# Optimization experiments

Hardware: AMD Instinct MI355X
Metric: run time of the kernel (lower is better)

Reference implementation:

```python
import jax, jax.numpy as jnp
import numpy as np

B, T, W, D = 2, 64, 32, 512
H = 8                      # n_heads
N = 64                     # d_state
EXPAND = 2
DIN = EXPAND * D           # 1024 d_inner
R = -(-D // 16)            # dt_rank = ceil(d_model/16) = 32
K = 4                      # d_conv (mamba default)


def setup_inputs():
    key = jax.random.key(0)
    ks = jax.random.split(key, 20)
    s = 0.02
    inp = {
        'x': jax.random.normal(ks[0], (B, T, W, D), jnp.float32),
        'wq': jax.random.normal(ks[1], (D, D), jnp.float32) * s,
        'bq': jnp.zeros((D,), jnp.float32),
        'wk': jax.random.normal(ks[2], (D, D), jnp.float32) * s,
        'bk': jnp.zeros((D,), jnp.float32),
        'wv': jax.random.normal(ks[3], (D, D), jnp.float32) * s,
        'bv': jnp.zeros((D,), jnp.float32),
        'wo': jax.random.normal(ks[4], (D, D), jnp.float32) * s,
        'bo': jnp.zeros((D,), jnp.float32),
        'in_proj_w': jax.random.normal(ks[5], (2 * DIN, D), jnp.float32) * s,
        'conv_w': jax.random.normal(ks[6], (DIN, 1, K), jnp.float32) * 0.2,
        'conv_b': jnp.zeros((DIN,), jnp.float32),
        'x_proj_w': jax.random.normal(ks[7], (R + 2 * N, DIN), jnp.float32) * s,
        'dt_proj_w': jax.random.normal(ks[8], (DIN, R), jnp.float32) * 0.1,
        'dt_proj_b': jnp.full((DIN,), -4.6, jnp.float32),  # ~softplus^-1(0.01)
        'A_log': jnp.log(jnp.broadcast_to(jnp.arange(1, N + 1, dtype=jnp.float32), (DIN, N))),
        'D_param': jnp.ones((DIN,), jnp.float32),
        'out_proj_w': jax.random.normal(ks[9], (D, DIN), jnp.float32) * s,
        'ln_w': jnp.ones((D,), jnp.float32),
        'ln_b': jnp.zeros((D,), jnp.float32),
    }
    return inp


def _attention(xf, wq, bq, wk, bk, wv, bv, wo, bo):
    b, L, d = xf.shape
    e = d // H
    q = (xf @ wq.T + bq).reshape(b, L, H, e)
    k = (xf @ wk.T + bk).reshape(b, L, H, e)
    v = (xf @ wv.T + bv).reshape(b, L, H, e)
    scale = 1.0 / jnp.sqrt(jnp.float32(e))
    scores = jnp.einsum('blhe,bshe->bhls', q, k) * scale
    causal = jnp.tril(jnp.ones((L, L), bool))
    scores = jnp.where(causal, scores, jnp.finfo(scores.dtype).min)
    attn = jax.nn.softmax(scores, axis=-1)  # dropout off (eval mode)
    out = jnp.einsum('bhls,bshe->blhe', attn, v).reshape(b, L, d)
    return out @ wo.T + bo


def _mamba(xf, in_proj_w, conv_w, conv_b, x_proj_w, dt_proj_w, dt_proj_b,
           A_log, D_param, out_proj_w):
    b, L, d = xf.shape
    xz = xf @ in_proj_w.T                 # (B,L,2*DIN)
    x_in, z = jnp.split(xz, 2, axis=-1)
    # causal depthwise conv1d over L
    xc = jnp.transpose(x_in, (0, 2, 1))   # (B,DIN,L)
    xc = jax.lax.conv_general_dilated(
        xc, conv_w, window_strides=(1,), padding=[(K - 1, 0)],
        feature_group_count=DIN, dimension_numbers=('NCH', 'OIH', 'NCH'))
    xc = xc + conv_b[None, :, None]
    u = jax.nn.silu(jnp.transpose(xc, (0, 2, 1)))   # (B,L,DIN)
    dbc = u @ x_proj_w.T                             # (B,L,R+2N)
    dt, Bm, Cm = dbc[..., :R], dbc[..., R:R + N], dbc[..., R + N:]
    dt = jax.nn.softplus(dt @ dt_proj_w.T + dt_proj_b)  # (B,L,DIN)
    A = -jnp.exp(A_log)                                 # (DIN,N)

    def step(h, t):
        dt_t, B_t, C_t, u_t = t  # (b,DIN),(b,N),(b,N),(b,DIN)
        dA = jnp.exp(dt_t[..., None] * A)                       # (b,DIN,N)
        h = dA * h + (dt_t * u_t)[..., None] * B_t[:, None, :]  # (b,DIN,N)
        y = jnp.einsum('bdn,bn->bd', h, C_t)
        return h, y

    h0 = jnp.zeros((b, DIN, N), xf.dtype)
    xs = (jnp.swapaxes(dt, 0, 1), jnp.swapaxes(Bm, 0, 1),
          jnp.swapaxes(Cm, 0, 1), jnp.swapaxes(u, 0, 1))
    _, ys = jax.lax.scan(step, h0, xs)
    y = jnp.swapaxes(ys, 0, 1) + u * D_param   # (B,L,DIN)
    y = y * jax.nn.silu(z)
    return y @ out_proj_w.T


def reference(x, wq, bq, wk, bk, wv, bv, wo, bo, in_proj_w, conv_w, conv_b,
              x_proj_w, dt_proj_w, dt_proj_b, A_log, D_param, out_proj_w,
              ln_w, ln_b):
    b, t, w, d = x.shape
    L = t * w
    xf = x.reshape(b, L, d)
    x_attn = _attention(xf, wq, bq, wk, bk, wv, bv, wo, bo).reshape(b, t, w, d)
    x_mamba = _mamba(xf, in_proj_w, conv_w, conv_b, x_proj_w, dt_proj_w,
                     dt_proj_b, A_log, D_param, out_proj_w).reshape(b, t, w, d)
    h = x + x_attn + x_mamba
    mu = jnp.mean(h, axis=-1, keepdims=True)
    var = jnp.mean(jnp.square(h - mu), axis=-1, keepdims=True)
    return (h - mu) * jax.lax.rsqrt(var + 1e-5) * ln_w + ln_b
```

## Files before the change

kernel.cpp:

```cpp
#include <hip/hip_runtime.h>

typedef __attribute__((ext_vector_type(4))) float f32x4;
typedef __attribute__((ext_vector_type(8))) short short8;
typedef __attribute__((ext_vector_type(2))) unsigned uint2e;

#define DEV static __device__ __forceinline__

DEV ushort f2b(float f) {
  union { float f; unsigned u; } v; v.f = f;
  unsigned r = v.u + 0x7FFF + ((v.u >> 16) & 1);
  return (ushort)(r >> 16);
}
DEV unsigned pack_bf2(float lo, float hi) {
  return (unsigned)f2b(lo) | ((unsigned)f2b(hi) << 16);
}
DEV float bflo(unsigned p) { return __uint_as_float(p << 16); }
DEV float bfhi(unsigned p) { return __uint_as_float(p & 0xFFFF0000u); }
DEV float b2f(ushort u) { return __uint_as_float((unsigned)u << 16); }

DEV float fexp2(float x) { float r; asm("v_exp_f32 %0, %1" : "=v"(r) : "v"(x)); return r; }

DEV float xor32_add_lo(float s) {
  uint2e r = __builtin_amdgcn_permlane32_swap(__float_as_uint(s), __float_as_uint(s), false, false);
  return s + __uint_as_float(r.x);
}

#define QP(x, ctrl) __int_as_float(__builtin_amdgcn_update_dpp(0, __float_as_int(x), (ctrl), 0xf, 0xf, false))
#define SWZ(x, off) __int_as_float(__builtin_amdgcn_ds_swizzle(__float_as_int(x), (off)))
#define DPP_ADD(x, ctrl, rmask) \
  ((x) + __int_as_float(__builtin_amdgcn_update_dpp(0, __float_as_int(x), (ctrl), (rmask), 0xf, false)))

#define LOG2E 1.44269504f

#define BB    2
#define LL    2048
#define DD    512
#define HH    8
#define EE    64
#define DIN   1024
#define NS    64
#define RR    32
#define BL    4096
#define NCH   16
#define TC    128
#define NC    1536
#define NQ    3584
#define XOFF  1536
#define ZOFF  2560
#define MFMA(a,b,c) __builtin_amdgcn_mfma_f32_16x16x32_bf16((a),(b),(c),0,0,0)

struct CvtJobs {
  const float* src[7];
  ushort*      dst[7];
  int          n[7];
};

__global__ __launch_bounds__(256) void cvt_multi(CvtJobs j) {
  int job = blockIdx.y;
  const float* s = j.src[job];
  ushort* d = j.dst[job];
  int n = j.n[job];
  for (int i = blockIdx.x * 256 + threadIdx.x; i < n; i += gridDim.x * 256)
    d[i] = f2b(s[i]);
}

__global__ __launch_bounds__(256) void pack_wcomb(
    const float* __restrict__ wo, const float* __restrict__ opw,
    const float* __restrict__ bq, const float* __restrict__ bk,
    const float* __restrict__ bv, ushort* __restrict__ wc,
    float* __restrict__ bqi)
{
  int i = blockIdx.x * 256 + threadIdx.x;
  if (i < NQ)
    bqi[i] = (i < DD) ? bq[i] : (i < 2 * DD) ? bk[i - DD] : (i < NC) ? bv[i - 2 * DD] : 0.f;
  if (i >= DD * NC) return;
  int n = i / NC, c = i - n * NC;
  float v = (c < DD) ? wo[n * DD + c] : opw[n * DIN + (c - DD)];
  wc[i] = f2b(v);
}

__global__ __launch_bounds__(256) void gemm_bt(
    const ushort* __restrict__ A, const ushort* __restrict__ W,
    const float* __restrict__ bias, float* __restrict__ outF,
    ushort* __restrict__ outB, int M, int N, int K, int act)
{
  __shared__ ushort As[64][40];
  __shared__ ushort Ws[64][40];
  int m0 = blockIdx.y * 64, n0 = blockIdx.x * 64;
  int tid = threadIdx.x, l = tid & 63, w = tid >> 6;
  int wm = (w >> 1) * 32, wn = (w & 1) * 32;
  int lr = l & 15, kl = (l >> 4) * 8;
  int srow = tid >> 2, sk = (tid & 3) * 8;
  f32x4 acc[2][2] = {};

  for (int k0 = 0; k0 < K; k0 += 32) {
    uint4 av = *(const uint4*)&A[(size_t)(m0 + srow) * K + k0 + sk];
    uint4 wv;
    if (n0 + srow < N) wv = *(const uint4*)&W[(size_t)(n0 + srow) * K + k0 + sk];
    else { wv.x = 0; wv.y = 0; wv.z = 0; wv.w = 0; }
    *(uint4*)&As[srow][sk] = av;
    *(uint4*)&Ws[srow][sk] = wv;
    __syncthreads();
    short8 a0 = *(const short8*)&As[wm + lr][kl];
    short8 a1 = *(const short8*)&As[wm + 16 + lr][kl];
    short8 b0 = *(const short8*)&Ws[wn + lr][kl];
    short8 b1 = *(const short8*)&Ws[wn + 16 + lr][kl];
    acc[0][0] = MFMA(a0, b0, acc[0][0]);
    acc[0][1] = MFMA(a0, b1, acc[0][1]);
    acc[1][0] = MFMA(a1, b0, acc[1][0]);
    acc[1][1] = MFMA(a1, b1, acc[1][1]);
    __syncthreads();
  }

  #pragma unroll
  for (int mi = 0; mi < 2; mi++)
    #pragma unroll
    for (int ni = 0; ni < 2; ni++) {
      int rbase = m0 + wm + mi * 16 + ((l >> 4) << 2);
      int col = n0 + wn + ni * 16 + lr;
      if (col < N) {
        float bval = bias ? bias[col] : 0.f;
        #pragma unroll
        for (int r = 0; r < 4; r++) {
          float v = acc[mi][ni][r] + bval;
          if (act == 1) v = (v > 20.f) ? v : log1pf(__expf(v));
          size_t o = (size_t)(rbase + r) * N + col;
          if (outF) outF[o] = v;
          if (outB) outB[o] = f2b(v);
        }
      }
    }
}

__global__ __launch_bounds__(256) void gemm128(
    const ushort* __restrict__ A, const ushort* __restrict__ W,
    const float* __restrict__ bias, float* __restrict__ outF,
    ushort* __restrict__ outB, int M, int N, int K)
{
  __shared__ ushort As[128][40];
  __shared__ ushort Ws[128][40];
  int tid = threadIdx.x, l = tid & 63, w = tid >> 6;
  int m0 = blockIdx.y * 128, n0 = blockIdx.x * 128;
  int wm = (w >> 1) * 64, wn = (w & 1) * 64;
  int lr = l & 15, kl = (l >> 4) * 8;
  int srow = tid >> 1, sk = (tid & 1) * 16;
  f32x4 acc[4][4] = {};

  const ushort* Ap = A + (size_t)(m0 + srow) * K + sk;
  const ushort* Wp = W + (size_t)(n0 + srow) * K + sk;

  for (int k0 = 0; k0 < K; k0 += 32) {
    uint4 a0 = *(const uint4*)(Ap);
    uint4 a1 = *(const uint4*)(Ap + 8);
    uint4 b0 = *(const uint4*)(Wp);
    uint4 b1 = *(const uint4*)(Wp + 8);
    __syncthreads();
    *(uint4*)&As[srow][sk]     = a0;
    *(uint4*)&As[srow][sk + 8] = a1;
    *(uint4*)&Ws[srow][sk]     = b0;
    *(uint4*)&Ws[srow][sk + 8] = b1;
    __syncthreads();
    short8 af[4], bf[4];
    #pragma unroll
    for (int mi = 0; mi < 4; mi++) af[mi] = *(const short8*)&As[wm + mi * 16 + lr][kl];
    #pragma unroll
    for (int ni = 0; ni < 4; ni++) bf[ni] = *(const short8*)&Ws[wn + ni * 16 + lr][kl];
    #pragma unroll
    for (int mi = 0; mi < 4; mi++)
      #pragma unroll
      for (int ni = 0; ni < 4; ni++)
        acc[mi][ni] = MFMA(af[mi], bf[ni], acc[mi][ni]);
    Ap += 32; Wp += 32;
  }

  #pragma unroll
  for (int mi = 0; mi < 4; mi++)
    #pragma unroll
    for (int ni = 0; ni < 4; ni++) {
      int rbase = m0 + wm + mi * 16 + ((l >> 4) << 2);
      int col = n0 + wn + ni * 16 + lr;
      float bval = bias ? bias[col] : 0.f;
      #pragma unroll
      for (int r = 0; r < 4; r++) {
        float v = acc[mi][ni][r] + bval;
        size_t o = (size_t)(rbase + r) * N + col;
        if (outF) outF[o] = v;
        if (outB) outB[o] = f2b(v);
      }
    }
}

__global__ __launch_bounds__(256) void attn_xproj(
    const ushort* __restrict__ qkv, ushort* __restrict__ comb,
    const ushort* __restrict__ ub, const ushort* __restrict__ xpw,
    float* __restrict__ dbc)
{
  __shared__ ushort smem[4 * 64 * 72];
  int id = blockIdx.x;
  int tid = threadIdx.x, l = tid & 63, w = tid >> 6;

  if (id < 512) {
    typedef ushort row72[72];
    row72* Qs = (row72*)smem;
    row72* Ks = Qs + 64;
    row72* Vt = Ks + 64;
    row72* Ps = Vt + 64;
    int qt = 31 - (id & 31), h = (id >> 5) & 7, b = id >> 8;
    int w16 = w * 16, lr = l & 15, kl = (l >> 4) * 8;

    for (int i = tid; i < 512; i += 256) {
      int row = i >> 3, c8 = (i & 7) * 8;
      *(uint4*)&Qs[row][c8] =
          *(const uint4*)&qkv[((size_t)(b * LL + qt * 64 + row)) * NQ + h * EE + c8];
    }
    __syncthreads();

    float l_r[4] = {0.f, 0.f, 0.f, 0.f};
    f32x4 oacc[4] = {};
    const float SSC = 0.125f * LOG2E;

    for (int kv = 0; kv <= qt; kv++) {
      for (int i = tid; i < 512; i += 256) {
        int s = i >> 3, c8 = (i & 7) * 8;
        size_t rb = ((size_t)(b * LL + kv * 64 + s)) * NQ + h * EE + c8;
        *(uint4*)&Ks[s][c8] = *(const uint4*)&qkv[rb + DD];
        uint4 vv = *(const uint4*)&qkv[rb + 2 * DD];
        const ushort* pv = (const ushort*)&vv;
        #pragma unroll
        for (int jj = 0; jj < 8; jj++) Vt[c8 + jj][s] = pv[jj];
      }
      __syncthreads();

      f32x4 sacc[4] = {};
      #pragma unroll
      for (int kk = 0; kk < 2; kk++) {
        short8 aq = *(const short8*)&Qs[w16 + lr][kk * 32 + kl];
        #pragma unroll
        for (int nt = 0; nt < 4; nt++) {
          short8 bk8 = *(const short8*)&Ks[nt * 16 + lr][kk * 32 + kl];
          sacc[nt] = MFMA(aq, bk8, sacc[nt]);
        }
      }

      bool diag = (kv == qt);
      #pragma unroll
      for (int r = 0; r < 4; r++) {
        int rloc = w16 + ((l >> 4) << 2) + r;
        float rs = 0.f;
        #pragma unroll
        for (int nt = 0; nt < 4; nt++) {
          float v = sacc[nt][r] * SSC;
          if (diag && (nt * 16 + lr) > rloc) v = -1e30f;
          float p = fexp2(v);
          rs += p;
          Ps[rloc][nt * 16 + lr] = f2b(p);
        }
        rs += QP(rs, 0xB1);
        rs += QP(rs, 0x4E);
        rs += SWZ(rs, 0x101F);
        rs += SWZ(rs, 0x201F);
        l_r[r] += rs;
      }

      #pragma unroll
      for (int kk = 0; kk < 2; kk++) {
        short8 ap = *(const short8*)&Ps[w16 + lr][kk * 32 + kl];
        #pragma unroll
        for (int nt = 0; nt < 4; nt++) {
          short8 bv8 = *(const short8*)&Vt[nt * 16 + lr][kk * 32 + kl];
          oacc[nt] = MFMA(ap, bv8, oacc[nt]);
        }
      }
      __syncthreads();
    }

    #pragma unroll
    for (int nt = 0; nt < 4; nt++)
      #pragma unroll
      for (int r = 0; r < 4; r++) {
        int row = qt * 64 + w16 + ((l >> 4) << 2) + r;
        float v = oacc[nt][r] / l_r[r];
        comb[((size_t)(b * LL + row)) * NC + h * EE + nt * 16 + lr] = f2b(v);
      }
  } else {
    typedef ushort row40[40];
    row40* As = (row40*)smem;
    row40* Ws = As + 64;
    int rid = id - 512;
    int n0 = (rid % 3) * 64, m0 = (rid / 3) * 64;
    int wm = (w >> 1) * 32, wn = (w & 1) * 32;
    int lr = l & 15, kl = (l >> 4) * 8;
    int srow = tid >> 2, sk = (tid & 3) * 8;
    f32x4 acc[2][2] = {};

    for (int k0 = 0; k0 < DIN; k0 += 32) {
      uint4 av = *(const uint4*)&ub[(size_t)(m0 + srow) * DIN + k0 + sk];
      uint4 wv;
      if (n0 + srow < 160) wv = *(const uint4*)&xpw[(size_t)(n0 + srow) * DIN + k0 + sk];
      else { wv.x = 0; wv.y = 0; wv.z = 0; wv.w = 0; }
      *(uint4*)&As[srow][sk] = av;
      *(uint4*)&Ws[srow][sk] = wv;
      __syncthreads();
      short8 a0 = *(const short8*)&As[wm + lr][kl];
      short8 a1 = *(const short8*)&As[wm + 16 + lr][kl];
      short8 b0 = *(const short8*)&Ws[wn + lr][kl];
      short8 b1 = *(const short8*)&Ws[wn + 16 + lr][kl];
      acc[0][0] = MFMA(a0, b0, acc[0][0]);
      acc[0][1] = MFMA(a0, b1, acc[0][1]);
      acc[1][0] = MFMA(a1, b0, acc[1][0]);
      acc[1][1] = MFMA(a1, b1, acc[1][1]);
      __syncthreads();
    }

    #pragma unroll
    for (int mi = 0; mi < 2; mi++)
      #pragma unroll
      for (int ni = 0; ni < 2; ni++) {
        int rbase = m0 + wm + mi * 16 + ((l >> 4) << 2);
        int col = n0 + wn + ni * 16 + lr;
        if (col < 160) {
          #pragma unroll
          for (int r = 0; r < 4; r++)
            dbc[(size_t)(rbase + r) * 160 + col] = acc[mi][ni][r];
        }
      }
  }
}

__global__ __launch_bounds__(256) void conv_silu(
    const ushort* __restrict__ xz, const float* __restrict__ cw,
    const float* __restrict__ cb, ushort* __restrict__ ub)
{
  int i = blockIdx.x * 256 + threadIdx.x;
  int d = i & (DIN - 1);
  int r = i >> 10;
  int t0 = (r & (LL / 8 - 1)) * 8;
  int b = r >> 8;
  float c0 = cw[d * 4], c1 = cw[d * 4 + 1], c2 = cw[d * 4 + 2], c3 = cw[d * 4 + 3];
  float bias = cb[d];
  float xw[11];
  #pragma unroll
  for (int j = 0; j < 3; j++) {
    int tt = t0 - 3 + j;
    xw[j] = (tt >= 0) ? b2f(xz[((size_t)(b * LL + tt)) * NQ + XOFF + d]) : 0.f;
  }
  #pragma unroll
  for (int j = 0; j < 8; j++)
    xw[3 + j] = b2f(xz[((size_t)(b * LL + t0 + j)) * NQ + XOFF + d]);
  size_t obase = (size_t)(b * LL + t0) * DIN + d;
  #pragma unroll
  for (int j = 0; j < 8; j++) {
    float s = bias + xw[j] * c0 + xw[j + 1] * c1 + xw[j + 2] * c2 + xw[j + 3] * c3;
    ub[obase + (size_t)j * DIN] = f2b(s / (1.f + __expf(-s)));
  }
}

__global__ __launch_bounds__(256) void dt_bc(
    const float* __restrict__ dbc, const ushort* __restrict__ dtw,
    const float* __restrict__ dtb, ushort* __restrict__ dt_b,
    unsigned* __restrict__ bbp, float4* __restrict__ bcp4)
{
  __shared__ ushort As[64][40];
  __shared__ ushort Ws[64][40];
  int id = blockIdx.x;
  int tid = threadIdx.x;
  if (id < 1024) {
    int m0 = (id >> 4) * 64, n0 = (id & 15) * 64;
    int l = tid & 63, w = tid >> 6;
    int wm = (w >> 1) * 32, wn = (w & 1) * 32;
    int lr = l & 15, kl = (l >> 4) * 8;
    int srow = tid >> 2, sk = (tid & 3) * 8;

    const float* ar = dbc + (size_t)(m0 + srow) * 160 + sk;
    short8 av;
    #pragma unroll
    for (int j = 0; j < 8; j++) ((ushort*)&av)[j] = f2b(ar[j]);
    *(short8*)&As[srow][sk] = av;
    *(uint4*)&Ws[srow][sk] = *(const uint4*)&dtw[(size_t)(n0 + srow) * RR + sk];
    __syncthreads();

    f32x4 acc[2][2] = {};
    short8 a0 = *(const short8*)&As[wm + lr][kl];
    short8 a1 = *(const short8*)&As[wm + 16 + lr][kl];
    short8 b0 = *(const short8*)&Ws[wn + lr][kl];
    short8 b1 = *(const short8*)&Ws[wn + 16 + lr][kl];
    acc[0][0] = MFMA(a0, b0, acc[0][0]);
    acc[0][1] = MFMA(a0, b1, acc[0][1]);
    acc[1][0] = MFMA(a1, b0, acc[1][0]);
    acc[1][1] = MFMA(a1, b1, acc[1][1]);

    #pragma unroll
    for (int mi = 0; mi < 2; mi++)
      #pragma unroll
      for (int ni = 0; ni < 2; ni++) {
        int rbase = m0 + wm + mi * 16 + ((l >> 4) << 2);
        int col = n0 + wn + ni * 16 + lr;
        float bval = dtb[col];
        #pragma unroll
        for (int r = 0; r < 4; r++) {
          float v = acc[mi][ni][r] + bval;
          v = (v > 20.f) ? v : log1pf(__expf(v));
          dt_b[(size_t)(rbase + r) * DIN + col] = f2b(v);
        }
      }
  } else {
    int i = (id - 1024) * 256 + tid;
    int n = i & 63, tp = (i >> 6) & 1023, b = i >> 16;
    size_t r0 = ((size_t)(b * LL + 2 * tp)) * 160;
    float B0 = dbc[r0 + 32 + n],  C0 = dbc[r0 + 96 + n];
    float B1 = dbc[r0 + 192 + n], C1 = dbc[r0 + 256 + n];
    bbp[i] = pack_bf2(B0, B1);
    bcp4[i] = make_float4(B0, C0, B1, C1);
  }
}

__global__ __launch_bounds__(256) void pack_dtu(
    const ushort* __restrict__ dtb16, const ushort* __restrict__ ub,
    const ushort* __restrict__ xz, const float* __restrict__ dpar,
    unsigned* __restrict__ dtu_p, unsigned* __restrict__ sg_p)
{
  __shared__ float s_dt[32][65], s_du[32][65], s_gz[32][65], s_ug[32][65];
  int d0 = blockIdx.x * 64, t0 = blockIdx.y * 32;
  int tid = threadIdx.x;
  int c = tid & 63, r4 = tid >> 6;
  float Dv = dpar[d0 + c];
  #pragma unroll
  for (int k = 0; k < 8; k++) {
    int r = k * 4 + r4;
    size_t row = (size_t)(t0 + r);
    float dtv = b2f(dtb16[row * DIN + d0 + c]);
    float uv  = b2f(ub   [row * DIN + d0 + c]);
    float zz  = b2f(xz   [row * NQ + ZOFF + d0 + c]);
    float g = zz / (1.f + __expf(-zz));
    s_dt[r][c] = dtv;
    s_du[r][c] = dtv * uv;
    s_gz[r][c] = g;
    s_ug[r][c] = uv * Dv * g;
  }
  __syncthreads();
  int dl = tid >> 2, q = tid & 3;
  int b = t0 >> 11, tl0 = t0 & (LL - 1);
  size_t obase = ((size_t)(b * DIN + d0 + dl)) * LL + tl0 + q * 8;
  #pragma unroll
  for (int tt = 0; tt < 8; tt++) {
    int t = q * 8 + tt;
    dtu_p[obase + tt] = pack_bf2(s_dt[t][dl], s_du[t][dl]);
    sg_p [obase + tt] = pack_bf2(s_gz[t][dl], s_ug[t][dl]);
  }
}

__global__ __launch_bounds__(256) void scan_phase1(
    const unsigned* __restrict__ dtu_p, const unsigned* __restrict__ bbp,
    const float* __restrict__ alog, float* __restrict__ hf, float* __restrict__ ap)
{
  __shared__ float lds[4][TC][2];
  int tid = threadIdx.x, w = tid >> 6, l = tid & 63;
  int wid = blockIdx.x * 4 + w;
  int d = wid & (DIN - 1);
  int c = (wid >> 10) & (NCH - 1);
  int b = wid >> 14;
  float An2 = -__expf(alog[d * NS + l]) * LOG2E;

  size_t pbase = ((size_t)(b * DIN + d)) * LL + c * TC;
  unsigned p0 = dtu_p[pbase + l];
  unsigned p1 = dtu_p[pbase + 64 + l];
  float s0 = bflo(p0), s1 = bflo(p1);
  s0 = DPP_ADD(s0, 0x111, 0xf); s0 = DPP_ADD(s0, 0x112, 0xf);
  s0 = DPP_ADD(s0, 0x114, 0xf); s0 = DPP_ADD(s0, 0x118, 0xf);
  s0 = DPP_ADD(s0, 0x142, 0xa); s0 = DPP_ADD(s0, 0x143, 0xc);
  s1 = DPP_ADD(s1, 0x111, 0xf); s1 = DPP_ADD(s1, 0x112, 0xf);
  s1 = DPP_ADD(s1, 0x114, 0xf); s1 = DPP_ADD(s1, 0x118, 0xf);
  s1 = DPP_ADD(s1, 0x142, 0xa); s1 = DPP_ADD(s1, 0x143, 0xc);
  float T0 = __uint_as_float(__builtin_amdgcn_readlane(__float_as_uint(s0), 63));
  float T  = T0 + __uint_as_float(__builtin_amdgcn_readlane(__float_as_uint(s1), 63));
  lds[w][l][0]      = T - s0;
  lds[w][l][1]      = bfhi(p0);
  lds[w][64 + l][0] = (T - T0) - s1;
  lds[w][64 + l][1] = bfhi(p1);
  __syncthreads();

  const unsigned* bq = bbp + ((size_t)(b * 1024 + c * 64) * 64 + l);
  float h0 = 0.f, h1 = 0.f;
  for (int g = 0; g < 16; g++) {
    unsigned bv[4];
    #pragma unroll
    for (int k = 0; k < 4; k++) bv[k] = bq[k * 64];
    const float* gb = &lds[w][g * 8][0];
    #pragma unroll
    for (int j = 0; j < 8; j++) {
      float2 dd = *(const float2*)(gb + j * 2);
      float Bv = (j & 1) ? bfhi(bv[j >> 1]) : bflo(bv[j >> 1]);
      float a = fexp2(dd.x * An2);
      if (j & 1) h1 += a * (dd.y * Bv);
      else       h0 += a * (dd.y * Bv);
    }
    bq += 256;
  }
  size_t o = (((size_t)((b << 10) + d) * NCH) + c) * 64 + l;
  hf[o] = h0 + h1;
  ap[o] = fexp2(T * An2);
}

__global__ __launch_bounds__(256) void scan_carry(
    const float* __restrict__ hf, const float* __restrict__ ap,
    float* __restrict__ carry)
{
  int i = blockIdx.x * 256 + threadIdx.x;
  int n = i & 63;
  int d = (i >> 6) & (DIN - 1);
  int b = i >> 16;
  size_t base = ((size_t)((b << 10) + d) * NCH) * 64 + n;
  float cur = 0.f;
  #pragma unroll
  for (int c = 0; c < NCH; c++) {
    carry[base + (size_t)c * 64] = cur;
    cur = ap[base + (size_t)c * 64] * cur + hf[base + (size_t)c * 64];
  }
}

__global__ __launch_bounds__(256) void scan_phase3(
    const unsigned* __restrict__ dtu_p, const unsigned* __restrict__ sg_p,
    const float4* __restrict__ bcp4, const float* __restrict__ alog,
    const float* __restrict__ carry, ushort* __restrict__ ymt)
{
  __shared__ float lds[4][TC][4];
  __shared__ ushort yt[4][TC];
  int tid = threadIdx.x, w = tid >> 6, l = tid & 63;
  int wid = blockIdx.x * 4 + w;
  int d = wid & (DIN - 1);
  int c = (wid >> 10) & (NCH - 1);
  int b = wid >> 14;
  float An2 = -__expf(alog[d * NS + l]) * LOG2E;

  size_t pbase = ((size_t)(b * DIN + d)) * LL + c * TC;
  #pragma unroll
  for (int q = 0; q < 2; q++) {
    unsigned pd = dtu_p[pbase + q * 64 + l];
    unsigned pg = sg_p [pbase + q * 64 + l];
    lds[w][q * 64 + l][0] = bflo(pd);
    lds[w][q * 64 + l][1] = bfhi(pd);
    lds[w][q * 64 + l][2] = bflo(pg);
    lds[w][q * 64 + l][3] = bfhi(pg);
  }
  __syncthreads();

  float h = carry[(((size_t)((b << 10) + d) * NCH) + c) * 64 + l];
  const float4* bq = bcp4 + ((size_t)(b * 1024 + c * 64) * 64 + l);
  bool s1f = l & 1, s2f = l & 2, s4f = l & 4;
  bool wl = l < 8;

  for (int g = 0; g < 16; g++) {
    float4 bcs[4];
    bcs[0] = bq[0]; bcs[1] = bq[64]; bcs[2] = bq[128]; bcs[3] = bq[192];
    const float* gb = &lds[w][g * 8][0];
    float p[8];
    #pragma unroll
    for (int j = 0; j < 8; j++) {
      float2 dd = *(const float2*)(gb + j * 4);
      float Bv = (j & 1) ? bcs[j >> 1].z : bcs[j >> 1].x;
      float Cv = (j & 1) ? bcs[j >> 1].w : bcs[j >> 1].y;
      float a = fexp2(dd.x * An2);
      h = a * h + dd.y * Bv;
      p[j] = h * Cv;
    }
    #pragma unroll
    for (int j = 0; j < 8; j++) p[j] += QP(p[j], 0xB1);
    float q0 = s1f ? p[1] : p[0];
    float q1 = s1f ? p[3] : p[2];
    float q2 = s1f ? p[5] : p[4];
    float q3 = s1f ? p[7] : p[6];
    q0 += QP(q0, 0x4E); q1 += QP(q1, 0x4E);
    q2 += QP(q2, 0x4E); q3 += QP(q3, 0x4E);
    float r0 = s2f ? q1 : q0;
    float r1 = s2f ? q3 : q2;
    r0 += SWZ(r0, 0x101F); r1 += SWZ(r1, 0x101F);
    float s = s4f ? r1 : r0;
    s += QP(s, 0x128);
    s += SWZ(s, 0x401F);
    s = xor32_add_lo(s);

    float2 sgv = *(const float2*)(&lds[w][g * 8 + (l & 7)][2]);
    if (wl) yt[w][g * 8 + l] = f2b(s * sgv.x + sgv.y);
    bq += 256;
  }
  __syncthreads();
  unsigned vv = *(const unsigned*)&yt[w][2 * l];
  ((unsigned*)(ymt + pbase))[l] = vv;
}

__global__ __launch_bounds__(256) void transpose_ym(
    const ushort* __restrict__ ymt, ushort* __restrict__ comb)
{
  __shared__ ushort tile[64][72];
  int tid = threadIdx.x;
  int bx = blockIdx.x;
  int by = blockIdx.y;
  int b  = blockIdx.z;
  int r = tid >> 2, c16 = (tid & 3) * 16;
  const ushort* src = ymt + ((size_t)(b * DIN + bx * 64 + r)) * LL + by * 64 + c16;
  *(uint4*)&tile[r][c16]     = *(const uint4*)src;
  *(uint4*)&tile[r][c16 + 8] = *(const uint4*)(src + 8);
  __syncthreads();
  ushort tmp[16];
  #pragma unroll
  for (int j = 0; j < 16; j++) tmp[j] = tile[c16 + j][r];
  ushort* dst = comb + ((size_t)(b * LL + by * 64 + r)) * NC + DD + bx * 64 + c16;
  *(uint4*)dst       = *(uint4*)&tmp[0];
  *(uint4*)(dst + 8) = *(uint4*)&tmp[8];
}

__global__ __launch_bounds__(256) void residual_ln(
    const float* __restrict__ x, const float* __restrict__ so,
    const float* __restrict__ lw, const float* __restrict__ lb,
    float* __restrict__ out)
{
  int row = blockIdx.x * 4 + (threadIdx.x >> 6);
  int l = threadIdx.x & 63;
  size_t base = (size_t)row * DD;
  float h[8];
  float s = 0.f, s2 = 0.f;
  #pragma unroll
  for (int half = 0; half < 2; half++) {
    int c = half * 256 + l * 4;
    float4 xv = *(const float4*)(x + base + c);
    float4 sv = *(const float4*)(so + base + c);
    float* hp = h + half * 4;
    hp[0] = xv.x + sv.x;
    hp[1] = xv.y + sv.y;
    hp[2] = xv.z + sv.z;
    hp[3] = xv.w + sv.w;
    #pragma unroll
    for (int j = 0; j < 4; j++) { s += hp[j]; s2 += hp[j] * hp[j]; }
  }
  #pragma unroll
  for (int o = 1; o < 64; o <<= 1) { s += __shfl_xor(s, o); s2 += __shfl_xor(s2, o); }
  float mean = s * (1.f / DD);
  float var = s2 * (1.f / DD) - mean * mean;
  float rs = rsqrtf(var + 1e-5f);
  #pragma unroll
  for (int half = 0; half < 2; half++) {
    int c = half * 256 + l * 4;
    float4 ov;
    ov.x = (h[half*4+0] - mean) * rs * lw[c+0] + lb[c+0];
    ov.y = (h[half*4+1] - mean) * rs * lw[c+1] + lb[c+1];
    ov.z = (h[half*4+2] - mean) * rs * lw[c+2] + lb[c+2];
    ov.w = (h[half*4+3] - mean) * rs * lw[c+3] + lb[c+3];
    *(float4*)(out + base + c) = ov;
  }
}

extern "C" void kernel_launch(void* const* d_in, const int* in_sizes, int n_in,
                              void* d_out, int out_size, void* d_ws, size_t ws_size,
                              hipStream_t stream) {
  const float* x    = (const float*)d_in[0];
  const float* wq   = (const float*)d_in[1];
  const float* bq   = (const float*)d_in[2];
  const float* wk   = (const float*)d_in[3];
  const float* bk   = (const float*)d_in[4];
  const float* wv   = (const float*)d_in[5];
  const float* bv   = (const float*)d_in[6];
  const float* wo   = (const float*)d_in[7];
  const float* bo   = (const float*)d_in[8];
  const float* inw  = (const float*)d_in[9];
  const float* cw   = (const float*)d_in[10];
  const float* cb   = (const float*)d_in[11];
  const float* xpw  = (const float*)d_in[12];
  const float* dtw  = (const float*)d_in[13];
  const float* dtb  = (const float*)d_in[14];
  const float* alog = (const float*)d_in[15];
  const float* dpar = (const float*)d_in[16];
  const float* opw  = (const float*)d_in[17];
  const float* lnw  = (const float*)d_in[18];
  const float* lnb  = (const float*)d_in[19];

  char* ws = (char*)d_ws;
  size_t off = 0;
  auto alloc = [&](size_t bytes) -> void* {
    void* p = ws + off;
    off += (bytes + 255) & ~(size_t)255;
    return p;
  };

  const size_t BLD = (size_t)BL * DD;
  const size_t BLDIN = (size_t)BL * DIN;

  ushort* xf_b   = (ushort*)alloc(BLD * 2);
  ushort* wqi_b  = (ushort*)alloc((size_t)NQ * DD * 2);
  float*  bqi    = (float*)alloc(NQ * 4);
  ushort* xpw_b  = (ushort*)alloc(160 * DIN * 2);
  ushort* dtw_b  = (ushort*)alloc(DIN * RR * 2);
  ushort* wcomb_b= (ushort*)alloc((size_t)DD * NC * 2);
  ushort* qkvxz_b= (ushort*)alloc((size_t)BL * NQ * 2);
  ushort* comb_a = (ushort*)alloc((size_t)BL * NC * 2);
  float*  sum_o  = (float*)alloc(BLD * 4);
  ushort* u_b    = (ushort*)alloc(BLDIN * 2);
  float*  dbc    = (float*)alloc((size_t)BL * 160 * 4);
  ushort* dt_b   = (ushort*)alloc(BLDIN * 2);
  ushort* ymt_b  = (ushort*)alloc(BLDIN * 2);
  unsigned* bbp  = (unsigned*)alloc((size_t)BB * (LL / 2) * NS * 4);
  float4* bcp4   = (float4*)alloc((size_t)BB * (LL / 2) * NS * sizeof(float4));
  unsigned* dtu_p = (unsigned*)alloc(BLDIN * 4);
  unsigned* sg_p  = (unsigned*)alloc(BLDIN * 4);

  const size_t SCN = (size_t)BB * DIN * NCH * 64;
  float* hf_s    = (float*)qkvxz_b;
  float* ap_s    = hf_s + SCN;
  float* carry_s = (float*)alloc(SCN * 4);

  CvtJobs cj;
  cj.src[0] = x;    cj.dst[0] = xf_b;                cj.n[0] = (int)BLD;
  cj.src[1] = wq;   cj.dst[1] = wqi_b;               cj.n[1] = DD * DD;
  cj.src[2] = wk;   cj.dst[2] = wqi_b + DD * DD;     cj.n[2] = DD * DD;
  cj.src[3] = wv;   cj.dst[3] = wqi_b + 2 * DD * DD; cj.n[3] = DD * DD;
  cj.src[4] = inw;  cj.dst[4] = wqi_b + 3 * DD * DD; cj.n[4] = 2 * DIN * DD;
  cj.src[5] = xpw;  cj.dst[5] = xpw_b;               cj.n[5] = 160 * DIN;
  cj.src[6] = dtw;  cj.dst[6] = dtw_b;               cj.n[6] = DIN * RR;
  cvt_multi<<<dim3(256, 7), 256, 0, stream>>>(cj);
  pack_wcomb<<<dim3((DD * NC + 255) / 256), 256, 0, stream>>>(wo, opw, bq, bk, bv, wcomb_b, bqi);

  gemm128<<<dim3(28, 32), 256, 0, stream>>>(xf_b, wqi_b, bqi, nullptr, qkvxz_b, BL, NQ, DD);

  conv_silu<<<dim3(2048), 256, 0, stream>>>(qkvxz_b, cw, cb, u_b);

  attn_xproj<<<dim3(704), 256, 0, stream>>>(qkvxz_b, comb_a, u_b, xpw_b, dbc);

  dt_bc<<<dim3(1536), 256, 0, stream>>>(dbc, dtw_b, dtb, dt_b, bbp, bcp4);

  pack_dtu<<<dim3(16, 128), 256, 0, stream>>>(dt_b, u_b, qkvxz_b, dpar, dtu_p, sg_p);
  scan_phase1<<<dim3(8192), 256, 0, stream>>>(dtu_p, bbp, alog, hf_s, ap_s);
  scan_carry<<<dim3(512), 256, 0, stream>>>(hf_s, ap_s, carry_s);
  scan_phase3<<<dim3(8192), 256, 0, stream>>>(dtu_p, sg_p, bcp4, alog, carry_s, ymt_b);
  transpose_ym<<<dim3(16, 32, BB), 256, 0, stream>>>(ymt_b, comb_a);

  gemm_bt<<<dim3(8, 64), 256, 0, stream>>>(comb_a, wcomb_b, bo, sum_o, nullptr, BL, DD, NC, 0);

  residual_ln<<<dim3(1024), 256, 0, stream>>>(x, sum_o, lnw, lnb, (float*)d_out);
}
```

Before: 346.3 us.

## Fuse dt packing into dt_bc GEMM and merge scan phase1 with carry

The dt projection kernel now packs dt, dt*u, the silu gate and the D-skip term directly from its tile through shared memory and writes the transposed packed buffers. This removes the separate pack_dtu kernel and the bf16 dt_b round trip. Scan phase 1 and the carry propagation are merged into one kernel per (batch, channel) that keeps chunk states in LDS, which drops the hf/ap global buffers and one launch. The trade-offs are lower parallelism in phase 1 (2048 blocks, each wave doing 4 chunks serially) and more LDS per block in dt_bc.

```diff
diff --git a/kernel.cpp b/kernel.cpp
--- a/kernel.cpp
+++ b/kernel.cpp
@@ -357,15 +357,20 @@
 
 __global__ __launch_bounds__(256) void dt_bc(
     const float* __restrict__ dbc, const ushort* __restrict__ dtw,
-    const float* __restrict__ dtb, ushort* __restrict__ dt_b,
+    const float* __restrict__ dtb, const float* __restrict__ dpar,
+    const ushort* __restrict__ ub, const ushort* __restrict__ xz,
+    unsigned* __restrict__ dtu_p, unsigned* __restrict__ sg_p,
     unsigned* __restrict__ bbp, float4* __restrict__ bcp4)
 {
   __shared__ ushort As[64][40];
   __shared__ ushort Ws[64][40];
+  __shared__ unsigned s_a[64][65];
+  __shared__ unsigned s_b[64][65];
   int id = blockIdx.x;
   int tid = threadIdx.x;
   if (id < 1024) {
     int m0 = (id >> 4) * 64, n0 = (id & 15) * 64;
+    int b = m0 >> 11, t0g = m0 & (LL - 1);
     int l = tid & 63, w = tid >> 6;
     int wm = (w >> 1) * 32, wn = (w & 1) * 32;
     int lr = l & 15, kl = (l >> 4) * 8;
@@ -393,16 +398,49 @@
     for (int mi = 0; mi < 2; mi++)
       #pragma unroll
       for (int ni = 0; ni < 2; ni++) {
-        int rbase = m0 + wm + mi * 16 + ((l >> 4) << 2);
-        int col = n0 + wn + ni * 16 + lr;
-        float bval = dtb[col];
+        int rl = wm + mi * 16 + ((l >> 4) << 2);
+        int cl = wn + ni * 16 + lr;
+        float bval = dtb[n0 + cl];
         #pragma unroll
         for (int r = 0; r < 4; r++) {
           float v = acc[mi][ni][r] + bval;
           v = (v > 20.f) ? v : log1pf(__expf(v));
-          dt_b[(size_t)(rbase + r) * DIN + col] = f2b(v);
+          s_a[rl + r][cl] = __float_as_uint(v);
         }
       }
+    __syncthreads();
+
+    {
+      int c = tid & 63, r4 = tid >> 6;
+      float Dv = dpar[n0 + c];
+      #pragma unroll
+      for (int k = 0; k < 16; k++) {
+        int r = k * 4 + r4;
+        float dtv = __uint_as_float(s_a[r][c]);
+        float uv  = b2f(ub[(size_t)(m0 + r) * DIN + n0 + c]);
+        float zz  = b2f(xz[(size_t)(m0 + r) * NQ + ZOFF + n0 + c]);
+        float g = zz / (1.f + __expf(-zz));
+        s_a[r][c] = pack_bf2(dtv, dtv * uv);
+        s_b[r][c] = pack_bf2(g, uv * Dv * g);
+      }
+    }
+    __syncthreads();
+
+    {
+      int dl = tid >> 2, q = tid & 3;
+      unsigned vd[16], vs[16];
+      #pragma unroll
+      for (int j = 0; j < 16; j++) {
+        vd[j] = s_a[q * 16 + j][dl];
+        vs[j] = s_b[q * 16 + j][dl];
+      }
+      size_t obase = ((size_t)(b * DIN + n0 + dl)) * LL + t0g + q * 16;
+      #pragma unroll
+      for (int jj = 0; jj < 4; jj++) {
+        *(uint4*)&dtu_p[obase + jj * 4] = *(uint4*)&vd[jj * 4];
+        *(uint4*)&sg_p [obase + jj * 4] = *(uint4*)&vs[jj * 4];
+      }
+    }
   } else {
     int i = (id - 1024) * 256 + tid;
     int n = i & 63, tp = (i >> 6) & 1023, b = i >> 16;
@@ -414,108 +452,70 @@
   }
 }
 
-__global__ __launch_bounds__(256) void pack_dtu(
-    const ushort* __restrict__ dtb16, const ushort* __restrict__ ub,
-    const ushort* __restrict__ xz, const float* __restrict__ dpar,
-    unsigned* __restrict__ dtu_p, unsigned* __restrict__ sg_p)
-{
-  __shared__ float s_dt[32][65], s_du[32][65], s_gz[32][65], s_ug[32][65];
-  int d0 = blockIdx.x * 64, t0 = blockIdx.y * 32;
-  int tid = threadIdx.x;
-  int c = tid & 63, r4 = tid >> 6;
-  float Dv = dpar[d0 + c];
-  #pragma unroll
-  for (int k = 0; k < 8; k++) {
-    int r = k * 4 + r4;
-    size_t row = (size_t)(t0 + r);
-    float dtv = b2f(dtb16[row * DIN + d0 + c]);
-    float uv  = b2f(ub   [row * DIN + d0 + c]);
-    float zz  = b2f(xz   [row * NQ + ZOFF + d0 + c]);
-    float g = zz / (1.f + __expf(-zz));
-    s_dt[r][c] = dtv;
-    s_du[r][c] = dtv * uv;
-    s_gz[r][c] = g;
-    s_ug[r][c] = uv * Dv * g;
+__global__ __launch_bounds__(256) void scan_p1c(
+    const unsigned* __restrict__ dtu_p, const unsigned* __restrict__ bbp,
+    const float* __restrict__ alog, float* __restrict__ carry)
+{
+  __shared__ float ldsE[4][TC][2];
+  __shared__ float hfL[NCH][NS];
+  __shared__ float apL[NCH][NS];
+  int tid = threadIdx.x, w = tid >> 6, l = tid & 63;
+  int bid = blockIdx.x;
+  int d = bid & (DIN - 1);
+  int b = bid >> 10;
+  float An2 = -__expf(alog[d * NS + l]) * LOG2E;
+
+  for (int k = 0; k < 4; k++) {
+    int cc = w * 4 + k;
+    size_t pbase = ((size_t)(b * DIN + d)) * LL + cc * TC;
+    unsigned p0 = dtu_p[pbase + l];
+    unsigned p1 = dtu_p[pbase + 64 + l];
+    float s0 = bflo(p0), s1 = bflo(p1);
+    s0 = DPP_ADD(s0, 0x111, 0xf); s0 = DPP_ADD(s0, 0x112, 0xf);
+    s0 = DPP_ADD(s0, 0x114, 0xf); s0 = DPP_ADD(s0, 0x118, 0xf);
+    s0 = DPP_ADD(s0, 0x142, 0xa); s0 = DPP_ADD(s0, 0x143, 0xc);
+    s1 = DPP_ADD(s1, 0x111, 0xf); s1 = DPP_ADD(s1, 0x112, 0xf);
+    s1 = DPP_ADD(s1, 0x114, 0xf); s1 = DPP_ADD(s1, 0x118, 0xf);
+    s1 = DPP_ADD(s1, 0x142, 0xa); s1 = DPP_ADD(s1, 0x143, 0xc);
+    float T0 = __uint_as_float(__builtin_amdgcn_readlane(__float_as_uint(s0), 63));
+    float T  = T0 + __uint_as_float(__builtin_amdgcn_readlane(__float_as_uint(s1), 63));
+    ldsE[w][l][0]      = T - s0;
+    ldsE[w][l][1]      = bfhi(p0);
+    ldsE[w][64 + l][0] = (T - T0) - s1;
+    ldsE[w][64 + l][1] = bfhi(p1);
+
+    const unsigned* bq = bbp + ((size_t)(b * 1024 + cc * 64) * 64 + l);
+    float h0 = 0.f, h1 = 0.f;
+    for (int g = 0; g < 16; g++) {
+      unsigned bv[4];
+      #pragma unroll
+      for (int kk = 0; kk < 4; kk++) bv[kk] = bq[kk * 64];
+      const float* gb = &ldsE[w][g * 8][0];
+      #pragma unroll
+      for (int j = 0; j < 8; j++) {
+        float2 dd = *(const float2*)(gb + j * 2);
+        float Bv = (j & 1) ? bfhi(bv[j >> 1]) : bflo(bv[j >> 1]);
+        float a = fexp2(dd.x * An2);
+        if (j & 1) h1 += a * (dd.y * Bv);
+        else       h0 += a * (dd.y * Bv);
+      }
+      bq += 256;
+    }
+    hfL[cc][l] = h0 + h1;
+    apL[cc][l] = fexp2(T * An2);
   }
   __syncthreads();
-  int dl = tid >> 2, q = tid & 3;
-  int b = t0 >> 11, tl0 = t0 & (LL - 1);
-  size_t obase = ((size_t)(b * DIN + d0 + dl)) * LL + tl0 + q * 8;
-  #pragma unroll
-  for (int tt = 0; tt < 8; tt++) {
-    int t = q * 8 + tt;
-    dtu_p[obase + tt] = pack_bf2(s_dt[t][dl], s_du[t][dl]);
-    sg_p [obase + tt] = pack_bf2(s_gz[t][dl], s_ug[t][dl]);
-  }
-}
-
-__global__ __launch_bounds__(256) void scan_phase1(
-    const unsigned* __restrict__ dtu_p, const unsigned* __restrict__ bbp,
-    const float* __restrict__ alog, float* __restrict__ hf, float* __restrict__ ap)
-{
-  __shared__ float lds[4][TC][2];
-  int tid = threadIdx.x, w = tid >> 6, l = tid & 63;
-  int wid = blockIdx.x * 4 + w;
-  int d = wid & (DIN - 1);
-  int c = (wid >> 10) & (NCH - 1);
-  int b = wid >> 14;
-  float An2 = -__expf(alog[d * NS + l]) * LOG2E;
-
-  size_t pbase = ((size_t)(b * DIN + d)) * LL + c * TC;
-  unsigned p0 = dtu_p[pbase + l];
-  unsigned p1 = dtu_p[pbase + 64 + l];
-  float s0 = bflo(p0), s1 = bflo(p1);
-  s0 = DPP_ADD(s0, 0x111, 0xf); s0 = DPP_ADD(s0, 0x112, 0xf);
-  s0 = DPP_ADD(s0, 0x114, 0xf); s0 = DPP_ADD(s0, 0x118, 0xf);
-  s0 = DPP_ADD(s0, 0x142, 0xa); s0 = DPP_ADD(s0, 0x143, 0xc);
-  s1 = DPP_ADD(s1, 0x111, 0xf); s1 = DPP_ADD(s1, 0x112, 0xf);
-  s1 = DPP_ADD(s1, 0x114, 0xf); s1 = DPP_ADD(s1, 0x118, 0xf);
-  s1 = DPP_ADD(s1, 0x142, 0xa); s1 = DPP_ADD(s1, 0x143, 0xc);
-  float T0 = __uint_as_float(__builtin_amdgcn_readlane(__float_as_uint(s0), 63));
-  float T  = T0 + __uint_as_float(__builtin_amdgcn_readlane(__float_as_uint(s1), 63));
-  lds[w][l][0]      = T - s0;
-  lds[w][l][1]      = bfhi(p0);
-  lds[w][64 + l][0] = (T - T0) - s1;
-  lds[w][64 + l][1] = bfhi(p1);
-  __syncthreads();
-
-  const unsigned* bq = bbp + ((size_t)(b * 1024 + c * 64) * 64 + l);
-  float h0 = 0.f, h1 = 0.f;
-  for (int g = 0; g < 16; g++) {
-    unsigned bv[4];
-    #pragma unroll
-    for (int k = 0; k < 4; k++) bv[k] = bq[k * 64];
-    const float* gb = &lds[w][g * 8][0];
-    #pragma unroll
-    for (int j = 0; j < 8; j++) {
-      float2 dd = *(const float2*)(gb + j * 2);
-      float Bv = (j & 1) ? bfhi(bv[j >> 1]) : bflo(bv[j >> 1]);
-      float a = fexp2(dd.x * An2);
-      if (j & 1) h1 += a * (dd.y * Bv);
-      else       h0 += a * (dd.y * Bv);
-    }
-    bq += 256;
-  }
-  size_t o = (((size_t)((b << 10) + d) * NCH) + c) * 64 + l;
-  hf[o] = h0 + h1;
-  ap[o] = fexp2(T * An2);
-}
-
-__global__ __launch_bounds__(256) void scan_carry(
-    const float* __restrict__ hf, const float* __restrict__ ap,
-    float* __restrict__ carry)
-{
-  int i = blockIdx.x * 256 + threadIdx.x;
-  int n = i & 63;
-  int d = (i >> 6) & (DIN - 1);
-  int b = i >> 16;
-  size_t base = ((size_t)((b << 10) + d) * NCH) * 64 + n;
-  float cur = 0.f;
-  #pragma unroll
-  for (int c = 0; c < NCH; c++) {
-    carry[base + (size_t)c * 64] = cur;
-    cur = ap[base + (size_t)c * 64] * cur + hf[base + (size_t)c * 64];
-  }
+
+  float cur = 0.f, myc[4];
+  #pragma unroll
+  for (int cc = 0; cc < NCH; cc++) {
+    if ((cc >> 2) == w) myc[cc & 3] = cur;
+    cur = apL[cc][l] * cur + hfL[cc][l];
+  }
+  size_t cbase = ((size_t)((b << 10) + d) * NCH) * 64 + l;
+  #pragma unroll
+  for (int k = 0; k < 4; k++)
+    carry[cbase + (size_t)(w * 4 + k) * 64] = myc[k];
 }
 
 __global__ __launch_bounds__(256) void scan_phase3(
@@ -695,16 +695,12 @@
   float*  sum_o  = (float*)alloc(BLD * 4);
   ushort* u_b    = (ushort*)alloc(BLDIN * 2);
   float*  dbc    = (float*)alloc((size_t)BL * 160 * 4);
-  ushort* dt_b   = (ushort*)alloc(BLDIN * 2);
   ushort* ymt_b  = (ushort*)alloc(BLDIN * 2);
   unsigned* bbp  = (unsigned*)alloc((size_t)BB * (LL / 2) * NS * 4);
   float4* bcp4   = (float4*)alloc((size_t)BB * (LL / 2) * NS * sizeof(float4));
   unsigned* dtu_p = (unsigned*)alloc(BLDIN * 4);
   unsigned* sg_p  = (unsigned*)alloc(BLDIN * 4);
-
   const size_t SCN = (size_t)BB * DIN * NCH * 64;
-  float* hf_s    = (float*)qkvxz_b;
-  float* ap_s    = hf_s + SCN;
   float* carry_s = (float*)alloc(SCN * 4);
 
   CvtJobs cj;
@@ -724,11 +720,10 @@
 
   attn_xproj<<<dim3(704), 256, 0, stream>>>(qkvxz_b, comb_a, u_b, xpw_b, dbc);
 
-  dt_bc<<<dim3(1536), 256, 0, stream>>>(dbc, dtw_b, dtb, dt_b, bbp, bcp4);
-
-  pack_dtu<<<dim3(16, 128), 256, 0, stream>>>(dt_b, u_b, qkvxz_b, dpar, dtu_p, sg_p);
-  scan_phase1<<<dim3(8192), 256, 0, stream>>>(dtu_p, bbp, alog, hf_s, ap_s);
-  scan_carry<<<dim3(512), 256, 0, stream>>>(hf_s, ap_s, carry_s);
+  dt_bc<<<dim3(1536), 256, 0, stream>>>(dbc, dtw_b, dtb, dpar, u_b, qkvxz_b,
+                                        dtu_p, sg_p, bbp, bcp4);
+
+  scan_p1c<<<dim3(BB * DIN), 256, 0, stream>>>(dtu_p, bbp, alog, carry_s);
   scan_phase3<<<dim3(8192), 256, 0, stream>>>(dtu_p, sg_p, bcp4, alog, carry_s, ymt_b);
   transpose_ym<<<dim3(16, 32, BB), 256, 0, stream>>>(ymt_b, comb_a);
 
```

After: 342.3 us. About the same (-1.2%).
